# Kernel tuning notes

Hardware: AMD Instinct MI355X
Metric: run time of the kernel (lower is better)

## Reference

```python
import jax, jax.numpy as jnp
import numpy as np

EPS = 1e-6  # cell eps
LN_EPS = 1e-5  # torch LayerNorm default


def layer_norm(x, gamma, beta):
    mu = jnp.mean(x, axis=-1, keepdims=True)
    var = jnp.mean(jnp.square(x - mu), axis=-1, keepdims=True)
    return (x - mu) * jax.lax.rsqrt(var + LN_EPS) * gamma + beta


def normalized_exp_gate(pre):
    centered = pre - jnp.mean(pre, axis=1, keepdims=True)
    e = jnp.exp(jnp.clip(centered, -5.0, 5.0))
    return e / (jnp.sum(e, axis=1, keepdims=True) + EPS)


def setup_inputs() -> dict:
    key = jax.random.key(0)
    B, Din, H = 8192, 512, 1024
    ks = jax.random.split(key, 16)
    std = 1.0 / np.sqrt(H)
    u = lambda k, shape: jax.random.uniform(k, shape, jnp.float32, -std, std)
    return {
        "x": jax.random.normal(ks[0], (B, Din), jnp.float32),
        "h_prev": jax.random.normal(ks[1], (B, H), jnp.float32),
        "c_prev": jax.random.normal(ks[2], (B, H), jnp.float32),
        "Wx": u(ks[3], (4 * H, Din)),
        "bx": u(ks[4], (4 * H,)),
        "Wh": u(ks[5], (4 * H, H)),
        "bh": u(ks[6], (4 * H,)),
        "ln_in_g": u(ks[7], (4 * H,)),
        "ln_in_b": u(ks[8], (4 * H,)),
        "ln_hu_g": u(ks[9], (4 * H,)),
        "ln_hu_b": u(ks[10], (4 * H,)),
        "ln_c_g": u(ks[11], (H,)),
        "ln_c_b": u(ks[12], (H,)),
        "ln_h_g": u(ks[13], (H,)),
        "ln_h_b": u(ks[14], (H,)),
    }


def reference(x, h_prev, c_prev, Wx, bx, Wh, bh,
              ln_in_g, ln_in_b, ln_hu_g, ln_hu_b,
              ln_c_g, ln_c_b, ln_h_g, ln_h_b):
    # dropout p=0 -> identity (eval mode)
    gates_x = layer_norm(x @ Wx.T + bx, ln_in_g, ln_in_b)      # [B, 4H]
    gates_h = layer_norm(h_prev @ Wh.T + bh, ln_hu_g, ln_hu_b)  # [B, 4H]
    gates = gates_x + gates_h
    i, f, g, o = jnp.split(gates, 4, axis=1)
    i = normalized_exp_gate(i)
    f = normalized_exp_gate(f)
    gate_sum = i + f
    i = i / (gate_sum + EPS)
    f = f / (gate_sum + EPS)
    c_tilde = jnp.tanh(g)
    c = layer_norm(f * c_prev + i * c_tilde, ln_c_g, ln_c_b)
    o = jax.nn.sigmoid(o)
    c_out = layer_norm(jnp.tanh(c), ln_h_g, ln_h_b)
    h = o * c_out
    return (h, c)
```

## Files before the change

kernel.cpp:

```cpp
#include <hip/hip_runtime.h>
#include <hip/hip_bf16.h>
#include <stdint.h>
#include <math.h>

#define EPS_CELL 1e-6f
#define LN_EPS   1e-5f

typedef short short8 __attribute__((ext_vector_type(8)));
typedef float f32x4 __attribute__((ext_vector_type(4)));
typedef unsigned short ushort;

__device__ __forceinline__ ushort f2bf(float f) {
    union { float f; uint32_t u; } v; v.f = f;
    uint32_t r = v.u + 0x7FFFu + ((v.u >> 16) & 1u);
    return (ushort)(r >> 16);
}
__device__ __forceinline__ float bfbits2f(uint32_t hi16_in_place) {
    union { uint32_t u; float f; } v; v.u = hi16_in_place;
    return v.f;
}

__device__ __forceinline__ float fexp(float x)  { return __builtin_amdgcn_exp2f(x * 1.4426950408889634f); }
__device__ __forceinline__ float frcp(float x)  { return __builtin_amdgcn_rcpf(x); }
__device__ __forceinline__ float frsq(float x)  { return __builtin_amdgcn_rsqf(x); }
__device__ __forceinline__ float ftanh(float x) {
    float xc = fminf(fmaxf(x, -15.f), 15.f);
    float t  = fexp(2.f * xc);
    return (t - 1.f) * frcp(t + 1.f);
}
__device__ __forceinline__ float fsigm(float x) { return frcp(1.f + fexp(-x)); }

__global__ __launch_bounds__(256) void cast_f32_bf16(const float* __restrict__ in,
                                                     ushort* __restrict__ out,
                                                     int n) {
    int i = (blockIdx.x * 256 + threadIdx.x) * 8;
    if (i >= n) return;
    const float4* p = (const float4*)(in + i);
    float4 a = p[0], b = p[1];
    uint4 r;
    r.x = (uint32_t)f2bf(a.x) | ((uint32_t)f2bf(a.y) << 16);
    r.y = (uint32_t)f2bf(a.z) | ((uint32_t)f2bf(a.w) << 16);
    r.z = (uint32_t)f2bf(b.x) | ((uint32_t)f2bf(b.y) << 16);
    r.w = (uint32_t)f2bf(b.z) | ((uint32_t)f2bf(b.w) << 16);
    *(uint4*)(out + i) = r;
}

#define BAR()        __builtin_amdgcn_s_barrier()
#define SPRIO(x)     __builtin_amdgcn_s_setprio(x)
#define WAIT_LGKM0() do { asm volatile("s_waitcnt lgkmcnt(0)" ::: "memory"); \
                          __builtin_amdgcn_sched_barrier(0); } while (0)
#define WAIT_VM6()   do { asm volatile("s_waitcnt vmcnt(6)" ::: "memory"); \
                          __builtin_amdgcn_sched_barrier(0); } while (0)
#define WAIT_VM0()   do { asm volatile("s_waitcnt vmcnt(0)" ::: "memory"); \
                          __builtin_amdgcn_sched_barrier(0); } while (0)

template<int K>
__global__ __launch_bounds__(512, 2) void gemm256_8ph(
        const ushort* __restrict__ Ag,
        const ushort* __restrict__ Bg,
        const float*  __restrict__ bias,
        ushort* __restrict__ C,
        int M, int GN) {
    constexpr int NT = K / 64;
    constexpr int NP = NT / 2;

    __shared__ ushort lds[65536];

    const int t    = threadIdx.x;
    const int lane = t & 63;
    const int w    = t >> 6;
    const int wr   = w >> 2;
    const int wc   = w & 3;
    const int ln   = lane & 15;
    const int hi   = lane >> 4;
    const int sx   = ln & 7;

    const int bid = blockIdx.x;
    const int wg  = (bid & 7) * 64 + (bid >> 3);
    const int n0  = (wg & 15) * 256;
    const int m0  = (wg >> 4) * 256;

    const int trow = t >> 3;
    const int scol = (((t & 7) ^ (trow & 7)) * 8);

#define STG_A(buf, j, kb) __builtin_amdgcn_global_load_lds( \
    (const __attribute__((address_space(1))) void*)(Ag + (size_t)(m0 + (j)*64 + trow) * K + (kb) + scol), \
    (__attribute__((address_space(3))) void*)(lds + (buf)*32768 + (j)*4096 + t*8), 16, 0, 0)
#define STG_B(buf, j, kb) __builtin_amdgcn_global_load_lds( \
    (const __attribute__((address_space(1))) void*)(Bg + (size_t)(n0 + (j)*64 + trow) * K + (kb) + scol), \
    (__attribute__((address_space(3))) void*)(lds + (buf)*32768 + 16384 + (j)*4096 + t*8), 16, 0, 0)

    const int ca0  = ((0 + hi) ^ sx) * 8;
    const int ca1  = ((4 + hi) ^ sx) * 8;
    const int arow = (wr * 16 + ln) * 64;
    const int brow = (wc * 16 + ln) * 64 + 16384;

    short8 af[2][4], bf0[2][2], bf1[2][2];
    f32x4  acc[8][4] = {};

#define LD_A(buf, mbase) do { _Pragma("unroll") for (int m = 0; m < 4; ++m) { \
    af[0][m] = *(const short8*)&lds[(buf)*32768 + arow + ((mbase)+m)*2048 + ca0]; \
    af[1][m] = *(const short8*)&lds[(buf)*32768 + arow + ((mbase)+m)*2048 + ca1]; } } while (0)
#define LD_B(dst, buf, nbase) do { _Pragma("unroll") for (int n = 0; n < 2; ++n) { \
    dst[0][n] = *(const short8*)&lds[(buf)*32768 + brow + ((nbase)+n)*4096 + ca0]; \
    dst[1][n] = *(const short8*)&lds[(buf)*32768 + brow + ((nbase)+n)*4096 + ca1]; } } while (0)
#define MMQ(mb, nb, B_) do { _Pragma("unroll") for (int kk = 0; kk < 2; ++kk) \
    _Pragma("unroll") for (int m = 0; m < 4; ++m) \
    _Pragma("unroll") for (int n = 0; n < 2; ++n) \
        acc[(mb)+m][(nb)+n] = __builtin_amdgcn_mfma_f32_16x16x32_bf16( \
            af[kk][m], B_[kk][n], acc[(mb)+m][(nb)+n], 0, 0, 0); } while (0)

    STG_B(0,0,0);  STG_B(0,1,0);
    STG_A(0,0,0);  STG_A(0,1,0);
    STG_B(0,2,0);  STG_B(0,3,0);
    STG_A(0,2,0);  STG_A(0,3,0);
    STG_B(1,0,64); STG_B(1,1,64);
    STG_A(1,0,64); STG_A(1,1,64);
    STG_B(1,2,64); STG_B(1,3,64);
    WAIT_VM6(); BAR();

    for (int p = 0; p < NP; ++p) {
        const int k1 = (2*p + 1) * 64;
        const int t2 = (2*p + 2 < NT) ? (2*p + 2) : (2*p);
        const int t3 = (2*p + 3 < NT) ? (2*p + 3) : (2*p + 1);
        const int k2 = t2 * 64, k3 = t3 * 64;

        LD_A(0, 0); LD_B(bf0, 0, 0);
        STG_A(1,2,k1); STG_A(1,3,k1);
        BAR(); WAIT_LGKM0();
        SPRIO(1); MMQ(0,0,bf0); SPRIO(0); BAR();
        LD_B(bf1, 0, 2);
        STG_B(0,0,k2); STG_B(0,1,k2);
        BAR(); WAIT_LGKM0();
        SPRIO(1); MMQ(0,2,bf1); SPRIO(0); BAR();
        LD_A(0, 4);
        STG_A(0,0,k2); STG_A(0,1,k2);
        BAR(); WAIT_LGKM0();
        SPRIO(1); MMQ(4,0,bf0); SPRIO(0); BAR();
        STG_B(0,2,k2); STG_B(0,3,k2);
        BAR();
        SPRIO(1); MMQ(4,2,bf1); SPRIO(0);
        WAIT_VM6(); BAR();
        LD_A(1, 0); LD_B(bf0, 1, 0);
        STG_A(0,2,k2); STG_A(0,3,k2);
        BAR(); WAIT_LGKM0();
        SPRIO(1); MMQ(0,0,bf0); SPRIO(0); BAR();
        LD_B(bf1, 1, 2);
        STG_B(1,0,k3); STG_B(1,1,k3);
        BAR(); WAIT_LGKM0();
        SPRIO(1); MMQ(0,2,bf1); SPRIO(0); BAR();
        LD_A(1, 4);
        STG_A(1,0,k3); STG_A(1,1,k3);
        BAR(); WAIT_LGKM0();
        SPRIO(1); MMQ(4,0,bf0); SPRIO(0); BAR();
        STG_B(1,2,k3); STG_B(1,3,k3);
        BAR();
        SPRIO(1); MMQ(4,2,bf1); SPRIO(0);
        WAIT_VM6(); BAR();
    }

    WAIT_VM0();
    BAR();
#pragma unroll
    for (int n = 0; n < 4; ++n) {
        int cl   = n * 64 + wc * 16 + ln;
        float bv = bias[n0 + cl];
#pragma unroll
        for (int m = 0; m < 8; ++m) {
#pragma unroll
            for (int r = 0; r < 4; ++r) {
                int row = m * 32 + wr * 16 + hi * 4 + r;
                int sc  = (cl & 7) + ((((cl >> 3) ^ (row & 7))) << 3);
                lds[row * 256 + sc] = f2bf(acc[m][n][r] + bv);
            }
        }
    }
    BAR();
    {
        const int rr = t >> 5;
        const int oc = (t & 31) * 8;
#pragma unroll
        for (int i = 0; i < 16; ++i) {
            int row = i * 16 + rr;
            int sc  = (((oc >> 3) ^ (row & 7)) << 3);
            uint4 vv = *(const uint4*)&lds[row * 256 + sc];
            *(uint4*)(C + (size_t)(m0 + row) * GN + n0 + oc) = vv;
        }
    }
#undef STG_A
#undef STG_B
#undef LD_A
#undef LD_B
#undef MMQ
}

template<int NV>
__device__ __forceinline__ void block_reduce_sum(float* v, float* sred) {
    const int lane = threadIdx.x & 63;
    const int w    = threadIdx.x >> 6;
#pragma unroll
    for (int i = 0; i < NV; ++i) {
        float s = v[i];
#pragma unroll
        for (int o = 32; o > 0; o >>= 1) s += __shfl_down(s, o, 64);
        if (lane == 0) sred[i * 4 + w] = s;
    }
    __syncthreads();
#pragma unroll
    for (int i = 0; i < NV; ++i)
        v[i] = sred[i * 4 + 0] + sred[i * 4 + 1] + sred[i * 4 + 2] + sred[i * 4 + 3];
    __syncthreads();
}

__global__ __launch_bounds__(256) void fused_cell(
        const ushort* __restrict__ U, const ushort* __restrict__ V,
        const float* __restrict__ c_prev,
        const float* __restrict__ g_in, const float* __restrict__ b_in,
        const float* __restrict__ g_hu, const float* __restrict__ b_hu,
        const float* __restrict__ g_c,  const float* __restrict__ b_c,
        const float* __restrict__ g_h,  const float* __restrict__ b_h,
        float* __restrict__ out_h, float* __restrict__ out_c) {
    __shared__ float sred[16];
    const int r = blockIdx.x;
    const int t = threadIdx.x;
    const size_t rowG = (size_t)r * 4096;
    const size_t rowH = (size_t)r * 1024;
    const int c0 = t * 4;

    float uq[4][4], vq[4][4];
#pragma unroll
    for (int q = 0; q < 4; ++q) {
        uint2 uu = *(const uint2*)(U + rowG + q * 1024 + c0);
        uint2 vv = *(const uint2*)(V + rowG + q * 1024 + c0);
        uq[q][0] = bfbits2f(uu.x << 16); uq[q][1] = bfbits2f(uu.x & 0xFFFF0000u);
        uq[q][2] = bfbits2f(uu.y << 16); uq[q][3] = bfbits2f(uu.y & 0xFFFF0000u);
        vq[q][0] = bfbits2f(vv.x << 16); vq[q][1] = bfbits2f(vv.x & 0xFFFF0000u);
        vq[q][2] = bfbits2f(vv.y << 16); vq[q][3] = bfbits2f(vv.y & 0xFFFF0000u);
    }

    float red[4] = {0.f, 0.f, 0.f, 0.f};
#pragma unroll
    for (int q = 0; q < 4; ++q)
#pragma unroll
        for (int j = 0; j < 4; ++j) {
            red[0] += uq[q][j]; red[1] += uq[q][j] * uq[q][j];
            red[2] += vq[q][j]; red[3] += vq[q][j] * vq[q][j];
        }
    block_reduce_sum<4>(red, sred);
    const float inv4096 = 1.f / 4096.f;
    float mu_u = red[0] * inv4096, mu_v = red[2] * inv4096;
    float rs_u = frsq(red[1] * inv4096 - mu_u * mu_u + LN_EPS);
    float rs_v = frsq(red[3] * inv4096 - mu_v * mu_v + LN_EPS);

    float gate[4][4];
#pragma unroll
    for (int q = 0; q < 4; ++q) {
        int idx = q * 1024 + c0;
        float4 gi_ = *(const float4*)(g_in + idx);
        float4 bi_ = *(const float4*)(b_in + idx);
        float4 gh_ = *(const float4*)(g_hu + idx);
        float4 bh_ = *(const float4*)(b_hu + idx);
        float gia[4] = {gi_.x, gi_.y, gi_.z, gi_.w};
        float bia[4] = {bi_.x, bi_.y, bi_.z, bi_.w};
        float gha[4] = {gh_.x, gh_.y, gh_.z, gh_.w};
        float bha[4] = {bh_.x, bh_.y, bh_.z, bh_.w};
#pragma unroll
        for (int j = 0; j < 4; ++j) {
            float zu = (uq[q][j] - mu_u) * rs_u;
            float zv = (vq[q][j] - mu_v) * rs_v;
            gate[q][j] = zu * gia[j] + bia[j] + zv * gha[j] + bha[j];
        }
    }

    red[0] = gate[0][0] + gate[0][1] + gate[0][2] + gate[0][3];
    red[1] = gate[1][0] + gate[1][1] + gate[1][2] + gate[1][3];
    block_reduce_sum<2>(red, sred);
    const float inv1024 = 1.f / 1024.f;
    float mi = red[0] * inv1024, mf = red[1] * inv1024;

    float ei[4], ef[4];
#pragma unroll
    for (int q = 0; q < 4; ++q) {
        ei[q] = fexp(fminf(fmaxf(gate[0][q] - mi, -5.f), 5.f));
        ef[q] = fexp(fminf(fmaxf(gate[1][q] - mf, -5.f), 5.f));
    }
    red[0] = ei[0] + ei[1] + ei[2] + ei[3];
    red[1] = ef[0] + ef[1] + ef[2] + ef[3];
    block_reduce_sum<2>(red, sred);
    float inv_si = frcp(red[0] + EPS_CELL);
    float inv_sf = frcp(red[1] + EPS_CELL);

    float4 cp4 = *(const float4*)(c_prev + rowH + c0);
    float cprev[4] = {cp4.x, cp4.y, cp4.z, cp4.w};

    float cpv[4];
#pragma unroll
    for (int q = 0; q < 4; ++q) {
        float in_ = ei[q] * inv_si;
        float fn_ = ef[q] * inv_sf;
        float den = frcp(in_ + fn_ + EPS_CELL);
        float i2 = in_ * den, f2 = fn_ * den;
        cpv[q] = f2 * cprev[q] + i2 * ftanh(gate[2][q]);
    }
    red[0] = cpv[0] + cpv[1] + cpv[2] + cpv[3];
    red[1] = cpv[0] * cpv[0] + cpv[1] * cpv[1] + cpv[2] * cpv[2] + cpv[3] * cpv[3];
    block_reduce_sum<2>(red, sred);
    float mu_c = red[0] * inv1024;
    float rs_c = frsq(red[1] * inv1024 - mu_c * mu_c + LN_EPS);

    float cv[4], th[4];
    {
        float4 gc4 = *(const float4*)(g_c + c0);
        float4 bc4 = *(const float4*)(b_c + c0);
        float gca[4] = {gc4.x, gc4.y, gc4.z, gc4.w};
        float bca[4] = {bc4.x, bc4.y, bc4.z, bc4.w};
#pragma unroll
        for (int q = 0; q < 4; ++q) {
            cv[q] = (cpv[q] - mu_c) * rs_c * gca[q] + bca[q];
            th[q] = ftanh(cv[q]);
        }
    }
    {
        float4 o; o.x = cv[0]; o.y = cv[1]; o.z = cv[2]; o.w = cv[3];
        *(float4*)(out_c + rowH + c0) = o;
    }
    red[0] = th[0] + th[1] + th[2] + th[3];
    red[1] = th[0] * th[0] + th[1] * th[1] + th[2] * th[2] + th[3] * th[3];
    block_reduce_sum<2>(red, sred);
    float mu_t = red[0] * inv1024;
    float rs_t = frsq(red[1] * inv1024 - mu_t * mu_t + LN_EPS);

    float hv[4];
    {
        float4 gh4 = *(const float4*)(g_h + c0);
        float4 bh4 = *(const float4*)(b_h + c0);
        float gha[4] = {gh4.x, gh4.y, gh4.z, gh4.w};
        float bha[4] = {bh4.x, bh4.y, bh4.z, bh4.w};
#pragma unroll
        for (int q = 0; q < 4; ++q) {
            float co = (th[q] - mu_t) * rs_t * gha[q] + bha[q];
            float so = fsigm(gate[3][q]);
            hv[q] = so * co;
        }
    }
    {
        float4 o; o.x = hv[0]; o.y = hv[1]; o.z = hv[2]; o.w = hv[3];
        *(float4*)(out_h + rowH + c0) = o;
    }
}

extern "C" void kernel_launch(void* const* d_in, const int* in_sizes, int n_in,
                              void* d_out, int out_size, void* d_ws, size_t ws_size,
                              hipStream_t stream) {
    const float* x       = (const float*)d_in[0];
    const float* h_prev  = (const float*)d_in[1];
    const float* c_prev  = (const float*)d_in[2];
    const float* Wx      = (const float*)d_in[3];
    const float* bx      = (const float*)d_in[4];
    const float* Wh      = (const float*)d_in[5];
    const float* bh      = (const float*)d_in[6];
    const float* ln_in_g = (const float*)d_in[7];
    const float* ln_in_b = (const float*)d_in[8];
    const float* ln_hu_g = (const float*)d_in[9];
    const float* ln_hu_b = (const float*)d_in[10];
    const float* ln_c_g  = (const float*)d_in[11];
    const float* ln_c_b  = (const float*)d_in[12];
    const float* ln_h_g  = (const float*)d_in[13];
    const float* ln_h_b  = (const float*)d_in[14];

    const int B = 8192, Din = 512, H = 1024, G = 4096;

    ushort* xb  = (ushort*)d_ws;
    ushort* hb  = xb  + (size_t)B * Din;
    ushort* wxb = hb  + (size_t)B * H;
    ushort* whb = wxb + (size_t)G * Din;
    ushort* U   = whb + (size_t)G * H;
    ushort* V   = U   + (size_t)B * G;

    cast_f32_bf16<<<(B * Din) / 2048, 256, 0, stream>>>(x, xb, B * Din);
    cast_f32_bf16<<<(B * H)   / 2048, 256, 0, stream>>>(h_prev, hb, B * H);
    cast_f32_bf16<<<(G * Din) / 2048, 256, 0, stream>>>(Wx, wxb, G * Din);
    cast_f32_bf16<<<(G * H)   / 2048, 256, 0, stream>>>(Wh, whb, G * H);

    gemm256_8ph<512> <<<dim3(512), 512, 0, stream>>>(xb, wxb, bx, U, B, G);
    gemm256_8ph<1024><<<dim3(512), 512, 0, stream>>>(hb, whb, bh, V, B, G);

    float* out_h = (float*)d_out;
    float* out_c = out_h + (size_t)B * H;
    fused_cell<<<B, 256, 0, stream>>>(U, V, c_prev,
                                      ln_in_g, ln_in_b, ln_hu_g, ln_hu_b,
                                      ln_c_g, ln_c_b, ln_h_g, ln_h_b,
                                      out_h, out_c);
}
```

Measured before the change: 226.9 us.

## Split Wh GEMM into two half launches with unpinned and pinned wait variants

Makes the wait macros templates so the GEMM can drop the memory clobber and sched_barrier pins, which gives the compiler freedom to reorder around waitcnts. Splits the K=1024 GEMM into two 256-block launches over the row halves, the first unpinned and the second pinned, with the workgroup swizzle generalized to gridDim. The unpinned variant risks the compiler moving LDS reads across the waits, and the extra launch adds overhead and tail effects. It looks like an experiment comparing the two schedules.

```diff
diff --git a/kernel.cpp b/kernel.cpp
--- a/kernel.cpp
+++ b/kernel.cpp
@@ -45,22 +45,33 @@
     *(uint4*)(out + i) = r;
 }
 
-#define BAR()        __builtin_amdgcn_s_barrier()
-#define SPRIO(x)     __builtin_amdgcn_s_setprio(x)
-#define WAIT_LGKM0() do { asm volatile("s_waitcnt lgkmcnt(0)" ::: "memory"); \
-                          __builtin_amdgcn_sched_barrier(0); } while (0)
-#define WAIT_VM6()   do { asm volatile("s_waitcnt vmcnt(6)" ::: "memory"); \
-                          __builtin_amdgcn_sched_barrier(0); } while (0)
-#define WAIT_VM0()   do { asm volatile("s_waitcnt vmcnt(0)" ::: "memory"); \
-                          __builtin_amdgcn_sched_barrier(0); } while (0)
-
-template<int K>
+#define BAR()    __builtin_amdgcn_s_barrier()
+#define SPRIO(x) __builtin_amdgcn_s_setprio(x)
+
+template<int PIN> __device__ __forceinline__ void wait_lgkm0() {
+    if constexpr (PIN) {
+        asm volatile("s_waitcnt lgkmcnt(0)" ::: "memory");
+        __builtin_amdgcn_sched_barrier(0);
+    } else {
+        asm volatile("s_waitcnt lgkmcnt(0)");
+    }
+}
+template<int PIN> __device__ __forceinline__ void wait_vm6() {
+    if constexpr (PIN) {
+        asm volatile("s_waitcnt vmcnt(6)" ::: "memory");
+        __builtin_amdgcn_sched_barrier(0);
+    } else {
+        asm volatile("s_waitcnt vmcnt(6)");
+    }
+}
+
+template<int K, int PIN>
 __global__ __launch_bounds__(512, 2) void gemm256_8ph(
         const ushort* __restrict__ Ag,
         const ushort* __restrict__ Bg,
         const float*  __restrict__ bias,
         ushort* __restrict__ C,
-        int M, int GN) {
+        int GN, int m_base) {
     constexpr int NT = K / 64;
     constexpr int NP = NT / 2;
 
@@ -76,9 +87,10 @@
     const int sx   = ln & 7;
 
     const int bid = blockIdx.x;
-    const int wg  = (bid & 7) * 64 + (bid >> 3);
+    const int cpx = gridDim.x >> 3;
+    const int wg  = (bid & 7) * cpx + (bid >> 3);
     const int n0  = (wg & 15) * 256;
-    const int m0  = (wg >> 4) * 256;
+    const int m0  = (wg >> 4) * 256 + m_base;
 
     const int trow = t >> 3;
     const int scol = (((t & 7) ^ (trow & 7)) * 8);
@@ -117,7 +129,7 @@
     STG_B(1,0,64); STG_B(1,1,64);
     STG_A(1,0,64); STG_A(1,1,64);
     STG_B(1,2,64); STG_B(1,3,64);
-    WAIT_VM6(); BAR();
+    wait_vm6<PIN>(); BAR();
 
     for (int p = 0; p < NP; ++p) {
         const int k1 = (2*p + 1) * 64;
@@ -127,39 +139,39 @@
 
         LD_A(0, 0); LD_B(bf0, 0, 0);
         STG_A(1,2,k1); STG_A(1,3,k1);
-        BAR(); WAIT_LGKM0();
+        BAR(); wait_lgkm0<PIN>();
         SPRIO(1); MMQ(0,0,bf0); SPRIO(0); BAR();
         LD_B(bf1, 0, 2);
         STG_B(0,0,k2); STG_B(0,1,k2);
-        BAR(); WAIT_LGKM0();
+        BAR(); wait_lgkm0<PIN>();
         SPRIO(1); MMQ(0,2,bf1); SPRIO(0); BAR();
         LD_A(0, 4);
         STG_A(0,0,k2); STG_A(0,1,k2);
-        BAR(); WAIT_LGKM0();
+        BAR(); wait_lgkm0<PIN>();
         SPRIO(1); MMQ(4,0,bf0); SPRIO(0); BAR();
         STG_B(0,2,k2); STG_B(0,3,k2);
         BAR();
         SPRIO(1); MMQ(4,2,bf1); SPRIO(0);
-        WAIT_VM6(); BAR();
+        wait_vm6<PIN>(); BAR();
         LD_A(1, 0); LD_B(bf0, 1, 0);
         STG_A(0,2,k2); STG_A(0,3,k2);
-        BAR(); WAIT_LGKM0();
+        BAR(); wait_lgkm0<PIN>();
         SPRIO(1); MMQ(0,0,bf0); SPRIO(0); BAR();
         LD_B(bf1, 1, 2);
         STG_B(1,0,k3); STG_B(1,1,k3);
-        BAR(); WAIT_LGKM0();
+        BAR(); wait_lgkm0<PIN>();
         SPRIO(1); MMQ(0,2,bf1); SPRIO(0); BAR();
         LD_A(1, 4);
         STG_A(1,0,k3); STG_A(1,1,k3);
-        BAR(); WAIT_LGKM0();
+        BAR(); wait_lgkm0<PIN>();
         SPRIO(1); MMQ(4,0,bf0); SPRIO(0); BAR();
         STG_B(1,2,k3); STG_B(1,3,k3);
         BAR();
         SPRIO(1); MMQ(4,2,bf1); SPRIO(0);
-        WAIT_VM6(); BAR();
-    }
-
-    WAIT_VM0();
+        wait_vm6<PIN>(); BAR();
+    }
+
+    asm volatile("s_waitcnt vmcnt(0)" ::: "memory");
     BAR();
 #pragma unroll
     for (int n = 0; n < 4; ++n) {
@@ -382,8 +394,10 @@
     cast_f32_bf16<<<(G * Din) / 2048, 256, 0, stream>>>(Wx, wxb, G * Din);
     cast_f32_bf16<<<(G * H)   / 2048, 256, 0, stream>>>(Wh, whb, G * H);
 
-    gemm256_8ph<512> <<<dim3(512), 512, 0, stream>>>(xb, wxb, bx, U, B, G);
-    gemm256_8ph<1024><<<dim3(512), 512, 0, stream>>>(hb, whb, bh, V, B, G);
+    gemm256_8ph<512, 0><<<dim3(512), 512, 0, stream>>>(xb, wxb, bx, U, G, 0);
+
+    gemm256_8ph<1024, 0><<<dim3(256), 512, 0, stream>>>(hb, whb, bh, V, G, 0);
+    gemm256_8ph<1024, 1><<<dim3(256), 512, 0, stream>>>(hb, whb, bh, V, G, 4096);
 
     float* out_h = (float*)d_out;
     float* out_c = out_h + (size_t)B * H;
```

Measured after the change: 233.4 us. 1.03x slower.

## Map one row per wavefront in cell kernel and split GEMMs into half launches

Applied to the files above, without the earlier changes.

The cell epilogue now gives each 64-lane wavefront a whole row, with 16 elements per lane. All layer-norm and gate reductions become wave shuffles, so the shared-memory block reductions and their barriers go away. Each GEMM is also split into two launches that cover half of M each, using an m_base offset and a grid-size-aware block swizzle. The split adds launch overhead and halves per-launch parallelism, while the per-lane register use in the cell kernel grows.

```diff
diff --git a/kernel.cpp b/kernel.cpp
--- a/kernel.cpp
+++ b/kernel.cpp
@@ -29,6 +29,12 @@
     return (t - 1.f) * frcp(t + 1.f);
 }
 __device__ __forceinline__ float fsigm(float x) { return frcp(1.f + fexp(-x)); }
+
+__device__ __forceinline__ float wred64(float s) {
+#pragma unroll
+    for (int m = 32; m > 0; m >>= 1) s += __shfl_xor(s, m, 64);
+    return s;
+}
 
 __global__ __launch_bounds__(256) void cast_f32_bf16(const float* __restrict__ in,
                                                      ushort* __restrict__ out,
@@ -60,7 +66,7 @@
         const ushort* __restrict__ Bg,
         const float*  __restrict__ bias,
         ushort* __restrict__ C,
-        int M, int GN) {
+        int GN, int m_base) {
     constexpr int NT = K / 64;
     constexpr int NP = NT / 2;
 
@@ -76,9 +82,10 @@
     const int sx   = ln & 7;
 
     const int bid = blockIdx.x;
-    const int wg  = (bid & 7) * 64 + (bid >> 3);
+    const int cpx = gridDim.x >> 3;
+    const int wg  = (bid & 7) * cpx + (bid >> 3);
     const int n0  = (wg & 15) * 256;
-    const int m0  = (wg >> 4) * 256;
+    const int m0  = (wg >> 4) * 256 + m_base;
 
     const int trow = t >> 3;
     const int scol = (((t & 7) ^ (trow & 7)) * 8);
@@ -194,25 +201,7 @@
 #undef MMQ
 }
 
-template<int NV>
-__device__ __forceinline__ void block_reduce_sum(float* v, float* sred) {
-    const int lane = threadIdx.x & 63;
-    const int w    = threadIdx.x >> 6;
-#pragma unroll
-    for (int i = 0; i < NV; ++i) {
-        float s = v[i];
-#pragma unroll
-        for (int o = 32; o > 0; o >>= 1) s += __shfl_down(s, o, 64);
-        if (lane == 0) sred[i * 4 + w] = s;
-    }
-    __syncthreads();
-#pragma unroll
-    for (int i = 0; i < NV; ++i)
-        v[i] = sred[i * 4 + 0] + sred[i * 4 + 1] + sred[i * 4 + 2] + sred[i * 4 + 3];
-    __syncthreads();
-}
-
-__global__ __launch_bounds__(256) void fused_cell(
+__global__ __launch_bounds__(256) void fused_cell_wave(
         const ushort* __restrict__ U, const ushort* __restrict__ V,
         const float* __restrict__ c_prev,
         const float* __restrict__ g_in, const float* __restrict__ b_in,
@@ -220,132 +209,148 @@
         const float* __restrict__ g_c,  const float* __restrict__ b_c,
         const float* __restrict__ g_h,  const float* __restrict__ b_h,
         float* __restrict__ out_h, float* __restrict__ out_c) {
-    __shared__ float sred[16];
-    const int r = blockIdx.x;
-    const int t = threadIdx.x;
-    const size_t rowG = (size_t)r * 4096;
-    const size_t rowH = (size_t)r * 1024;
-    const int c0 = t * 4;
-
-    float uq[4][4], vq[4][4];
+    const int lane = threadIdx.x & 63;
+    const int row  = blockIdx.x * 4 + (threadIdx.x >> 6);
+    const size_t rowG = (size_t)row * 4096;
+    const size_t rowH = (size_t)row * 1024;
+    const int e0 = lane * 16;
+
+    uint4 up[4][2], vp[4][2];
 #pragma unroll
     for (int q = 0; q < 4; ++q) {
-        uint2 uu = *(const uint2*)(U + rowG + q * 1024 + c0);
-        uint2 vv = *(const uint2*)(V + rowG + q * 1024 + c0);
-        uq[q][0] = bfbits2f(uu.x << 16); uq[q][1] = bfbits2f(uu.x & 0xFFFF0000u);
-        uq[q][2] = bfbits2f(uu.y << 16); uq[q][3] = bfbits2f(uu.y & 0xFFFF0000u);
-        vq[q][0] = bfbits2f(vv.x << 16); vq[q][1] = bfbits2f(vv.x & 0xFFFF0000u);
-        vq[q][2] = bfbits2f(vv.y << 16); vq[q][3] = bfbits2f(vv.y & 0xFFFF0000u);
-    }
-
-    float red[4] = {0.f, 0.f, 0.f, 0.f};
+        const uint4* pu = (const uint4*)(U + rowG + q * 1024 + e0);
+        const uint4* pv = (const uint4*)(V + rowG + q * 1024 + e0);
+        up[q][0] = pu[0]; up[q][1] = pu[1];
+        vp[q][0] = pv[0]; vp[q][1] = pv[1];
+    }
+
+    float su = 0.f, squ = 0.f, sv = 0.f, sqv = 0.f;
 #pragma unroll
     for (int q = 0; q < 4; ++q)
 #pragma unroll
-        for (int j = 0; j < 4; ++j) {
-            red[0] += uq[q][j]; red[1] += uq[q][j] * uq[q][j];
-            red[2] += vq[q][j]; red[3] += vq[q][j] * vq[q][j];
-        }
-    block_reduce_sum<4>(red, sred);
+        for (int hw = 0; hw < 2; ++hw) {
+            uint32_t uw[4] = {up[q][hw].x, up[q][hw].y, up[q][hw].z, up[q][hw].w};
+            uint32_t vw[4] = {vp[q][hw].x, vp[q][hw].y, vp[q][hw].z, vp[q][hw].w};
+#pragma unroll
+            for (int j = 0; j < 4; ++j) {
+                float a0 = bfbits2f(uw[j] << 16), a1 = bfbits2f(uw[j] & 0xFFFF0000u);
+                float b0 = bfbits2f(vw[j] << 16), b1 = bfbits2f(vw[j] & 0xFFFF0000u);
+                su += a0 + a1; squ += a0 * a0 + a1 * a1;
+                sv += b0 + b1; sqv += b0 * b0 + b1 * b1;
+            }
+        }
+    su = wred64(su); squ = wred64(squ); sv = wred64(sv); sqv = wred64(sqv);
     const float inv4096 = 1.f / 4096.f;
-    float mu_u = red[0] * inv4096, mu_v = red[2] * inv4096;
-    float rs_u = frsq(red[1] * inv4096 - mu_u * mu_u + LN_EPS);
-    float rs_v = frsq(red[3] * inv4096 - mu_v * mu_v + LN_EPS);
-
-    float gate[4][4];
+    float mu_u = su * inv4096, mu_v = sv * inv4096;
+    float rs_u = frsq(squ * inv4096 - mu_u * mu_u + LN_EPS);
+    float rs_v = frsq(sqv * inv4096 - mu_v * mu_v + LN_EPS);
+
+    float gt[4][16];
 #pragma unroll
     for (int q = 0; q < 4; ++q) {
-        int idx = q * 1024 + c0;
-        float4 gi_ = *(const float4*)(g_in + idx);
-        float4 bi_ = *(const float4*)(b_in + idx);
-        float4 gh_ = *(const float4*)(g_hu + idx);
-        float4 bh_ = *(const float4*)(b_hu + idx);
-        float gia[4] = {gi_.x, gi_.y, gi_.z, gi_.w};
-        float bia[4] = {bi_.x, bi_.y, bi_.z, bi_.w};
-        float gha[4] = {gh_.x, gh_.y, gh_.z, gh_.w};
-        float bha[4] = {bh_.x, bh_.y, bh_.z, bh_.w};
-#pragma unroll
-        for (int j = 0; j < 4; ++j) {
-            float zu = (uq[q][j] - mu_u) * rs_u;
-            float zv = (vq[q][j] - mu_v) * rs_v;
-            gate[q][j] = zu * gia[j] + bia[j] + zv * gha[j] + bha[j];
-        }
-    }
-
-    red[0] = gate[0][0] + gate[0][1] + gate[0][2] + gate[0][3];
-    red[1] = gate[1][0] + gate[1][1] + gate[1][2] + gate[1][3];
-    block_reduce_sum<2>(red, sred);
+        float uf[16], vf[16];
+#pragma unroll
+        for (int hw = 0; hw < 2; ++hw) {
+            uint32_t uw[4] = {up[q][hw].x, up[q][hw].y, up[q][hw].z, up[q][hw].w};
+            uint32_t vw[4] = {vp[q][hw].x, vp[q][hw].y, vp[q][hw].z, vp[q][hw].w};
+#pragma unroll
+            for (int j = 0; j < 4; ++j) {
+                uf[hw * 8 + 2 * j]     = bfbits2f(uw[j] << 16);
+                uf[hw * 8 + 2 * j + 1] = bfbits2f(uw[j] & 0xFFFF0000u);
+                vf[hw * 8 + 2 * j]     = bfbits2f(vw[j] << 16);
+                vf[hw * 8 + 2 * j + 1] = bfbits2f(vw[j] & 0xFFFF0000u);
+            }
+        }
+        const int idx = q * 1024 + e0;
+#pragma unroll
+        for (int b4 = 0; b4 < 4; ++b4) {
+            float4 ga = *(const float4*)(g_in + idx + b4 * 4);
+            float4 ba = *(const float4*)(b_in + idx + b4 * 4);
+            float4 gb = *(const float4*)(g_hu + idx + b4 * 4);
+            float4 bb = *(const float4*)(b_hu + idx + b4 * 4);
+            gt[q][b4*4+0] = (uf[b4*4+0]-mu_u)*rs_u*ga.x + ba.x + (vf[b4*4+0]-mu_v)*rs_v*gb.x + bb.x;
+            gt[q][b4*4+1] = (uf[b4*4+1]-mu_u)*rs_u*ga.y + ba.y + (vf[b4*4+1]-mu_v)*rs_v*gb.y + bb.y;
+            gt[q][b4*4+2] = (uf[b4*4+2]-mu_u)*rs_u*ga.z + ba.z + (vf[b4*4+2]-mu_v)*rs_v*gb.z + bb.z;
+            gt[q][b4*4+3] = (uf[b4*4+3]-mu_u)*rs_u*ga.w + ba.w + (vf[b4*4+3]-mu_v)*rs_v*gb.w + bb.w;
+        }
+    }
+
+    float si = 0.f, sf = 0.f;
+#pragma unroll
+    for (int j = 0; j < 16; ++j) { si += gt[0][j]; sf += gt[1][j]; }
+    si = wred64(si); sf = wred64(sf);
     const float inv1024 = 1.f / 1024.f;
-    float mi = red[0] * inv1024, mf = red[1] * inv1024;
-
-    float ei[4], ef[4];
-#pragma unroll
-    for (int q = 0; q < 4; ++q) {
-        ei[q] = fexp(fminf(fmaxf(gate[0][q] - mi, -5.f), 5.f));
-        ef[q] = fexp(fminf(fmaxf(gate[1][q] - mf, -5.f), 5.f));
-    }
-    red[0] = ei[0] + ei[1] + ei[2] + ei[3];
-    red[1] = ef[0] + ef[1] + ef[2] + ef[3];
-    block_reduce_sum<2>(red, sred);
-    float inv_si = frcp(red[0] + EPS_CELL);
-    float inv_sf = frcp(red[1] + EPS_CELL);
-
-    float4 cp4 = *(const float4*)(c_prev + rowH + c0);
-    float cprev[4] = {cp4.x, cp4.y, cp4.z, cp4.w};
-
-    float cpv[4];
-#pragma unroll
-    for (int q = 0; q < 4; ++q) {
-        float in_ = ei[q] * inv_si;
-        float fn_ = ef[q] * inv_sf;
+    float mi = si * inv1024, mf = sf * inv1024;
+
+    float ei[16], ef[16];
+    float sei = 0.f, sef = 0.f;
+#pragma unroll
+    for (int j = 0; j < 16; ++j) {
+        ei[j] = fexp(fminf(fmaxf(gt[0][j] - mi, -5.f), 5.f));
+        ef[j] = fexp(fminf(fmaxf(gt[1][j] - mf, -5.f), 5.f));
+        sei += ei[j]; sef += ef[j];
+    }
+    sei = wred64(sei); sef = wred64(sef);
+    float inv_si = frcp(sei + EPS_CELL);
+    float inv_sf = frcp(sef + EPS_CELL);
+
+    float cp[16];
+#pragma unroll
+    for (int b4 = 0; b4 < 4; ++b4) {
+        float4 c4 = *(const float4*)(c_prev + rowH + e0 + b4 * 4);
+        cp[b4*4+0] = c4.x; cp[b4*4+1] = c4.y; cp[b4*4+2] = c4.z; cp[b4*4+3] = c4.w;
+    }
+    float cpv[16];
+    float sc = 0.f, sc2 = 0.f;
+#pragma unroll
+    for (int j = 0; j < 16; ++j) {
+        float in_ = ei[j] * inv_si;
+        float fn_ = ef[j] * inv_sf;
         float den = frcp(in_ + fn_ + EPS_CELL);
-        float i2 = in_ * den, f2 = fn_ * den;
-        cpv[q] = f2 * cprev[q] + i2 * ftanh(gate[2][q]);
-    }
-    red[0] = cpv[0] + cpv[1] + cpv[2] + cpv[3];
-    red[1] = cpv[0] * cpv[0] + cpv[1] * cpv[1] + cpv[2] * cpv[2] + cpv[3] * cpv[3];
-    block_reduce_sum<2>(red, sred);
-    float mu_c = red[0] * inv1024;
-    float rs_c = frsq(red[1] * inv1024 - mu_c * mu_c + LN_EPS);
-
-    float cv[4], th[4];
-    {
-        float4 gc4 = *(const float4*)(g_c + c0);
-        float4 bc4 = *(const float4*)(b_c + c0);
+        cpv[j] = fn_ * den * cp[j] + in_ * den * ftanh(gt[2][j]);
+        sc += cpv[j]; sc2 += cpv[j] * cpv[j];
+    }
+    sc = wred64(sc); sc2 = wred64(sc2);
+    float mu_c = sc * inv1024;
+    float rs_c = frsq(sc2 * inv1024 - mu_c * mu_c + LN_EPS);
+
+    float cv[16], th[16];
+    float st = 0.f, st2 = 0.f;
+#pragma unroll
+    for (int b4 = 0; b4 < 4; ++b4) {
+        float4 gc4 = *(const float4*)(g_c + e0 + b4 * 4);
+        float4 bc4 = *(const float4*)(b_c + e0 + b4 * 4);
         float gca[4] = {gc4.x, gc4.y, gc4.z, gc4.w};
         float bca[4] = {bc4.x, bc4.y, bc4.z, bc4.w};
 #pragma unroll
-        for (int q = 0; q < 4; ++q) {
-            cv[q] = (cpv[q] - mu_c) * rs_c * gca[q] + bca[q];
-            th[q] = ftanh(cv[q]);
-        }
-    }
-    {
-        float4 o; o.x = cv[0]; o.y = cv[1]; o.z = cv[2]; o.w = cv[3];
-        *(float4*)(out_c + rowH + c0) = o;
-    }
-    red[0] = th[0] + th[1] + th[2] + th[3];
-    red[1] = th[0] * th[0] + th[1] * th[1] + th[2] * th[2] + th[3] * th[3];
-    block_reduce_sum<2>(red, sred);
-    float mu_t = red[0] * inv1024;
-    float rs_t = frsq(red[1] * inv1024 - mu_t * mu_t + LN_EPS);
-
-    float hv[4];
-    {
-        float4 gh4 = *(const float4*)(g_h + c0);
-        float4 bh4 = *(const float4*)(b_h + c0);
+        for (int j = 0; j < 4; ++j) {
+            int k = b4 * 4 + j;
+            cv[k] = (cpv[k] - mu_c) * rs_c * gca[j] + bca[j];
+            th[k] = ftanh(cv[k]);
+            st += th[k]; st2 += th[k] * th[k];
+        }
+        float4 o; o.x = cv[b4*4+0]; o.y = cv[b4*4+1]; o.z = cv[b4*4+2]; o.w = cv[b4*4+3];
+        *(float4*)(out_c + rowH + e0 + b4 * 4) = o;
+    }
+    st = wred64(st); st2 = wred64(st2);
+    float mu_t = st * inv1024;
+    float rs_t = frsq(st2 * inv1024 - mu_t * mu_t + LN_EPS);
+
+#pragma unroll
+    for (int b4 = 0; b4 < 4; ++b4) {
+        float4 gh4 = *(const float4*)(g_h + e0 + b4 * 4);
+        float4 bh4 = *(const float4*)(b_h + e0 + b4 * 4);
         float gha[4] = {gh4.x, gh4.y, gh4.z, gh4.w};
         float bha[4] = {bh4.x, bh4.y, bh4.z, bh4.w};
-#pragma unroll
-        for (int q = 0; q < 4; ++q) {
-            float co = (th[q] - mu_t) * rs_t * gha[q] + bha[q];
-            float so = fsigm(gate[3][q]);
-            hv[q] = so * co;
-        }
-    }
-    {
+        float hv[4];
+#pragma unroll
+        for (int j = 0; j < 4; ++j) {
+            int k = b4 * 4 + j;
+            float co = (th[k] - mu_t) * rs_t * gha[j] + bha[j];
+            hv[j] = fsigm(gt[3][k]) * co;
+        }
         float4 o; o.x = hv[0]; o.y = hv[1]; o.z = hv[2]; o.w = hv[3];
-        *(float4*)(out_h + rowH + c0) = o;
+        *(float4*)(out_h + rowH + e0 + b4 * 4) = o;
     }
 }
 
@@ -382,13 +387,15 @@
     cast_f32_bf16<<<(G * Din) / 2048, 256, 0, stream>>>(Wx, wxb, G * Din);
     cast_f32_bf16<<<(G * H)   / 2048, 256, 0, stream>>>(Wh, whb, G * H);
 
-    gemm256_8ph<512> <<<dim3(512), 512, 0, stream>>>(xb, wxb, bx, U, B, G);
-    gemm256_8ph<1024><<<dim3(512), 512, 0, stream>>>(hb, whb, bh, V, B, G);
+    gemm256_8ph<512> <<<dim3(256), 512, 0, stream>>>(xb, wxb, bx, U, G, 0);
+    gemm256_8ph<512> <<<dim3(256), 512, 0, stream>>>(xb, wxb, bx, U, G, 4096);
+    gemm256_8ph<1024><<<dim3(256), 512, 0, stream>>>(hb, whb, bh, V, G, 0);
+    gemm256_8ph<1024><<<dim3(256), 512, 0, stream>>>(hb, whb, bh, V, G, 4096);
 
     float* out_h = (float*)d_out;
     float* out_c = out_h + (size_t)B * H;
-    fused_cell<<<B, 256, 0, stream>>>(U, V, c_prev,
-                                      ln_in_g, ln_in_b, ln_hu_g, ln_hu_b,
-                                      ln_c_g, ln_c_b, ln_h_g, ln_h_b,
-                                      out_h, out_c);
-}
+    fused_cell_wave<<<B / 4, 256, 0, stream>>>(U, V, c_prev,
+                                               ln_in_g, ln_in_b, ln_hu_g, ln_hu_b,
+                                               ln_c_g, ln_c_b, ln_h_g, ln_h_b,
+                                               out_h, out_c);
+}
```

After: 248.9 us. 1.1x slower.
